# Performance work log

Hardware: AMD Instinct MI355X
Metric: run time of the kernel (lower is better)

Reference implementation:

```python
import jax, jax.numpy as jnp
import numpy as np

K = 9      # kernel_size
H = 6      # num_head
HD = 64    # head_dim
D = H * HD # reduced_hidden_dim = 384
B, S = 16, 1024
OUT = 384  # hidden_dim // 2


def setup_inputs() -> dict:
    key = jax.random.key(0)
    k = jax.random.split(key, 5)
    q = jax.random.normal(k[0], (B, S, D), dtype=jnp.float32)
    ks = jax.random.normal(k[1], (B, S, D), dtype=jnp.float32)
    v = jax.random.normal(k[2], (B, S, D), dtype=jnp.float32)
    Wk = jax.random.normal(k[3], (K * H, D), dtype=jnp.float32) * 0.02
    bk = jnp.zeros((K * H,), dtype=jnp.float32)
    Wp = jax.random.normal(k[4], (OUT, D), dtype=jnp.float32) * 0.02
    bp = jnp.zeros((OUT,), dtype=jnp.float32)
    return {"q": q, "ks": ks, "v": v, "Wk": Wk, "bk": bk, "Wp": Wp, "bp": bp}


def reference(q, ks, v, Wk, bk, Wp, bp):
    b, s, d = v.shape
    pad = K // 2
    # expand4conv: zero-pad along seq and gather K-wide sliding windows
    vp = jnp.pad(v, ((0, 0), (pad, pad), (0, 0)))            # [B, S+K-1, D]
    win = jnp.stack([vp[:, i:i + s] for i in range(K)], -1)  # [B, S, D, K]
    win = win.reshape(b, s, H, HD, K)                        # [B, S, H, HD, K]
    # dynamic kernel: softmax over kernel taps
    logits = jnp.einsum('bsd,od->bso', q * ks, Wk) + bk       # [B, S, K*H]
    dk = jax.nn.softmax(logits.reshape(b, s, H, K), axis=-1)  # [B, S, H, K]
    # local weighted reduction over the window
    out = jnp.einsum('bshdk,bshk->bshd', win, dk).reshape(b, s, d)
    return jnp.einsum('bsd,od->bso', out, Wp) + bp            # [B, S, OUT]
```

## Files before the change

kernel.cpp:

```cpp
#include <hip/hip_runtime.h>
#include <hip/hip_bf16.h>

#define BB 16
#define SS 1024
#define DD 384
#define HH 6
#define KK 9
#define KH 54
#define OUTD 384
#define NKT 12
#define VLD 392
#define RPB 32
#define NTH 512

typedef __attribute__((ext_vector_type(4))) float floatx4;
typedef __attribute__((ext_vector_type(8))) __bf16 bf16x8;
typedef __attribute__((ext_vector_type(4))) __bf16 bf16x4;

__global__ __launch_bounds__(256) void cast_kernel(const float* __restrict__ Wk,
                                                   const float* __restrict__ Wp,
                                                   __bf16* __restrict__ WkT,
                                                   __bf16* __restrict__ WpT) {
    int i = blockIdx.x * 256 + threadIdx.x;
    if (i < 4 * NKT * 64 * 8) {
        int e = i & 7, lane = (i >> 3) & 63, t = i >> 9;
        int kstep = t % NKT, ntile = t / NKT;
        int row = ntile * 16 + (lane & 15);
        int col = kstep * 32 + ((lane >> 4) << 3) + e;
        WkT[i] = (row < KH) ? (__bf16)Wk[row * DD + col] : (__bf16)0.0f;
    } else if (i < 24576 + 24 * NKT * 64 * 8) {
        int j = i - 24576;
        int e = j & 7, lane = (j >> 3) & 63, t = j >> 9;
        int kstep = t % NKT, ntile = t / NKT;
        int row = ntile * 16 + (lane & 15);
        int col = kstep * 32 + ((lane >> 4) << 3) + e;
        WpT[j] = (__bf16)Wp[row * DD + col];
    }
}

__global__ __launch_bounds__(NTH, 4) void fused_kernel(const float* __restrict__ q,
                                                       const float* __restrict__ ks,
                                                       const float* __restrict__ v,
                                                       const __bf16* __restrict__ WkT,
                                                       const float* __restrict__ bk,
                                                       const __bf16* __restrict__ WpT,
                                                       const float* __restrict__ bp,
                                                       float* __restrict__ out) {
    __shared__ __bf16 vqS[40 * VLD];
    __shared__ float  dkS[RPB * 56];
    __shared__ __align__(16) char uS[RPB * VLD * 2];
    float*  lgS = (float*)uS;
    __bf16* aS  = (__bf16*)uS;

    const int tid  = threadIdx.x;
    const int wave = tid >> 6;
    const int lane = tid & 63;
    const int m0   = blockIdx.x * RPB;
    const int b    = blockIdx.x >> 5;
    const int s0   = (blockIdx.x & 31) * RPB;
    const int fr   = lane & 15;
    const int fk   = (lane >> 4) * 8;
    const int col_in = lane & 15;
    const int rgrp   = (lane >> 4) * 4;

    floatx4 qv[6], kv[6], vpre[8];
    {
        const float* qb = q  + (size_t)m0 * DD;
        const float* kb = ks + (size_t)m0 * DD;
#pragma unroll
        for (int it = 0; it < 6; ++it) {
            int c = tid + it * NTH;
            int row = c / 96, col = (c % 96) * 4;
            qv[it] = *reinterpret_cast<const floatx4*>(qb + (size_t)row * DD + col);
            kv[it] = *reinterpret_cast<const floatx4*>(kb + (size_t)row * DD + col);
        }
        const float* vb = v + (size_t)b * SS * DD;
#pragma unroll
        for (int it = 0; it < 8; ++it) {
            int c = tid + it * NTH;
            int row = c / 96, col = (c % 96) * 4;
            int r = s0 + row - 4;
            int rc = r < 0 ? 0 : (r > SS - 1 ? SS - 1 : r);
            vpre[it] = *reinterpret_cast<const floatx4*>(vb + (size_t)rc * DD + col);
        }
#pragma unroll
        for (int it = 0; it < 6; ++it) {
            int c = tid + it * NTH;
            int row = c / 96, col = (c % 96) * 4;
            floatx4 pr = qv[it] * kv[it];
            bf16x4 pk = { (__bf16)pr.x, (__bf16)pr.y, (__bf16)pr.z, (__bf16)pr.w };
            *reinterpret_cast<bf16x4*>(&vqS[row * VLD + col]) = pk;
        }
    }
    __syncthreads();

    {
        const int rt = wave >> 2;
        const int nt = wave & 3;
        const __bf16* wkb = WkT + (((nt * NKT) * 64 + lane) << 3);
        bf16x8 wf0 = *reinterpret_cast<const bf16x8*>(wkb);
        bf16x8 wf1;
        floatx4 acc = {};
#pragma unroll
        for (int s = 0; s < NKT; ++s) {
            if (s + 1 < NKT) {
                const __bf16* nb = wkb + ((size_t)(s + 1) << 9);
                if ((s & 1) == 0) wf1 = *reinterpret_cast<const bf16x8*>(nb);
                else              wf0 = *reinterpret_cast<const bf16x8*>(nb);
            }
            bf16x8 af = *reinterpret_cast<const bf16x8*>(
                &vqS[(rt * 16 + fr) * VLD + s * 32 + fk]);
            acc = __builtin_amdgcn_mfma_f32_16x16x32_bf16(
                af, (s & 1) == 0 ? wf0 : wf1, acc, 0, 0, 0);
        }
#pragma unroll
        for (int r = 0; r < 4; ++r)
            lgS[(rt * 16 + rgrp + r) * 66 + nt * 16 + col_in] = acc[r];
    }
    __syncthreads();

    if (tid < RPB * HH) {
        int row = tid / HH, h = tid % HH;
        float lg[KK];
        float mx = -1e30f;
#pragma unroll
        for (int k = 0; k < KK; ++k) {
            float s = lgS[row * 66 + h * KK + k] + bk[h * KK + k];
            lg[k] = s;
            mx = fmaxf(mx, s);
        }
        float sum = 0.0f;
#pragma unroll
        for (int k = 0; k < KK; ++k) { lg[k] = __expf(lg[k] - mx); sum += lg[k]; }
        float inv = 1.0f / sum;
#pragma unroll
        for (int k = 0; k < KK; ++k) dkS[row * 56 + h * KK + k] = lg[k] * inv;
    }

    {
#pragma unroll
        for (int it = 0; it < 8; ++it) {
            int c = tid + it * NTH;
            if (c < 3840) {
                int row = c / 96, col = (c % 96) * 4;
                int r = s0 + row - 4;
                floatx4 val = vpre[it];
                if (r < 0 || r >= SS) val = floatx4{0.0f, 0.0f, 0.0f, 0.0f};
                bf16x4 vk = { (__bf16)val.x, (__bf16)val.y, (__bf16)val.z, (__bf16)val.w };
                *reinterpret_cast<bf16x4*>(&vqS[row * VLD + col]) = vk;
            }
        }
    }
    __syncthreads();

#pragma unroll
    for (int it = 0; it < 6; ++it) {
        int p = tid + it * NTH;
        int row = p / 96, c4 = p % 96;
        int h = c4 >> 4;
        const float* dkr = &dkS[row * 56 + h * KK];
        floatx4 a = {};
#pragma unroll
        for (int k = 0; k < KK; ++k) {
            bf16x4 w = *reinterpret_cast<const bf16x4*>(&vqS[(row + k) * VLD + c4 * 4]);
            floatx4 wf = { (float)w[0], (float)w[1], (float)w[2], (float)w[3] };
            a += wf * dkr[k];
        }
        bf16x4 o = { (__bf16)a.x, (__bf16)a.y, (__bf16)a.z, (__bf16)a.w };
        *reinterpret_cast<bf16x4*>(&aS[row * VLD + c4 * 4]) = o;
    }

    const int nt0 = wave * 3;
    const __bf16* wpb = WpT + (((nt0 * NKT) * 64 + lane) << 3);
    bf16x8 bfr[2][3];
#pragma unroll
    for (int j = 0; j < 3; ++j)
        bfr[0][j] = *reinterpret_cast<const bf16x8*>(wpb + ((size_t)(j * NKT) << 9));
    __syncthreads();

    {
        floatx4 acc[2][3] = {};
#pragma unroll
        for (int s = 0; s < NKT; ++s) {
            const int cur = s & 1, nxt = cur ^ 1;
            if (s + 1 < NKT) {
#pragma unroll
                for (int j = 0; j < 3; ++j)
                    bfr[nxt][j] = *reinterpret_cast<const bf16x8*>(
                        wpb + ((size_t)(j * NKT + s + 1) << 9));
            }
            bf16x8 a0 = *reinterpret_cast<const bf16x8*>(&aS[fr * VLD + s * 32 + fk]);
            bf16x8 a1 = *reinterpret_cast<const bf16x8*>(&aS[(16 + fr) * VLD + s * 32 + fk]);
#pragma unroll
            for (int j = 0; j < 3; ++j) {
                acc[0][j] = __builtin_amdgcn_mfma_f32_16x16x32_bf16(a0, bfr[cur][j], acc[0][j], 0, 0, 0);
                acc[1][j] = __builtin_amdgcn_mfma_f32_16x16x32_bf16(a1, bfr[cur][j], acc[1][j], 0, 0, 0);
            }
        }
        float* ob = out + (size_t)m0 * OUTD;
#pragma unroll
        for (int j = 0; j < 3; ++j) {
            int col = (nt0 + j) * 16 + col_in;
            float bv = bp[col];
#pragma unroll
            for (int rt = 0; rt < 2; ++rt)
#pragma unroll
                for (int r = 0; r < 4; ++r)
                    ob[(size_t)(rt * 16 + rgrp + r) * OUTD + col] = acc[rt][j][r] + bv;
        }
    }
}

extern "C" void kernel_launch(void* const* d_in, const int* in_sizes, int n_in,
                              void* d_out, int out_size, void* d_ws, size_t ws_size,
                              hipStream_t stream) {
    const float* q  = (const float*)d_in[0];
    const float* ks = (const float*)d_in[1];
    const float* v  = (const float*)d_in[2];
    const float* Wk = (const float*)d_in[3];
    const float* bk = (const float*)d_in[4];
    const float* Wp = (const float*)d_in[5];
    const float* bp = (const float*)d_in[6];
    float* out = (float*)d_out;

    __bf16* WkT = (__bf16*)d_ws;
    __bf16* WpT = (__bf16*)((char*)d_ws + 49152);

    cast_kernel<<<(24576 + 147456 + 255) / 256, 256, 0, stream>>>(Wk, Wp, WkT, WpT);
    fused_kernel<<<(BB * SS) / RPB, NTH, 0, stream>>>(q, ks, v, WkT, bk, WpT, bp, out);
}
```

Measured before the change: 122.9 us.

## Cut shared memory and registers to double occupancy of fused kernel

The q*ks product is now computed directly from global memory in MFMA fragment layout instead of being staged through shared memory. The v window is loaded and stored to LDS up front, with no register prefetch held across phases. Softmax weights reuse the logits buffer, and the local reduction results stay in registers until the v buffer can be overwritten. Together with launch bounds raised from 4 to 8 blocks per CU, this aims to cut LDS and VGPR use so more blocks fit per CU, at the cost of an extra barrier and less coalesced q/ks reads.

```diff
diff --git a/kernel.cpp b/kernel.cpp
--- a/kernel.cpp
+++ b/kernel.cpp
@@ -38,7 +38,7 @@
     }
 }
 
-__global__ __launch_bounds__(NTH, 4) void fused_kernel(const float* __restrict__ q,
+__global__ __launch_bounds__(NTH, 8) void fused_kernel(const float* __restrict__ q,
                                                        const float* __restrict__ ks,
                                                        const float* __restrict__ v,
                                                        const __bf16* __restrict__ WkT,
@@ -46,11 +46,8 @@
                                                        const __bf16* __restrict__ WpT,
                                                        const float* __restrict__ bp,
                                                        float* __restrict__ out) {
-    __shared__ __bf16 vqS[40 * VLD];
-    __shared__ float  dkS[RPB * 56];
-    __shared__ __align__(16) char uS[RPB * VLD * 2];
-    float*  lgS = (float*)uS;
-    __bf16* aS  = (__bf16*)uS;
+    __shared__ __bf16 vS[40 * VLD];
+    __shared__ float  lgS[RPB * 66];
 
     const int tid  = threadIdx.x;
     const int wave = tid >> 6;
@@ -63,40 +60,28 @@
     const int col_in = lane & 15;
     const int rgrp   = (lane >> 4) * 4;
 
-    floatx4 qv[6], kv[6], vpre[8];
     {
-        const float* qb = q  + (size_t)m0 * DD;
-        const float* kb = ks + (size_t)m0 * DD;
-#pragma unroll
-        for (int it = 0; it < 6; ++it) {
-            int c = tid + it * NTH;
-            int row = c / 96, col = (c % 96) * 4;
-            qv[it] = *reinterpret_cast<const floatx4*>(qb + (size_t)row * DD + col);
-            kv[it] = *reinterpret_cast<const floatx4*>(kb + (size_t)row * DD + col);
-        }
         const float* vb = v + (size_t)b * SS * DD;
 #pragma unroll
         for (int it = 0; it < 8; ++it) {
             int c = tid + it * NTH;
-            int row = c / 96, col = (c % 96) * 4;
-            int r = s0 + row - 4;
-            int rc = r < 0 ? 0 : (r > SS - 1 ? SS - 1 : r);
-            vpre[it] = *reinterpret_cast<const floatx4*>(vb + (size_t)rc * DD + col);
-        }
-#pragma unroll
-        for (int it = 0; it < 6; ++it) {
-            int c = tid + it * NTH;
-            int row = c / 96, col = (c % 96) * 4;
-            floatx4 pr = qv[it] * kv[it];
-            bf16x4 pk = { (__bf16)pr.x, (__bf16)pr.y, (__bf16)pr.z, (__bf16)pr.w };
-            *reinterpret_cast<bf16x4*>(&vqS[row * VLD + col]) = pk;
-        }
-    }
-    __syncthreads();
+            if (c < 3840) {
+                int row = c / 96, col = (c % 96) * 4;
+                int r = s0 + row - 4;
+                int rc = r < 0 ? 0 : (r > SS - 1 ? SS - 1 : r);
+                floatx4 val = *reinterpret_cast<const floatx4*>(vb + (size_t)rc * DD + col);
+                if (r < 0 || r >= SS) val = floatx4{0.0f, 0.0f, 0.0f, 0.0f};
+                bf16x4 vk4 = { (__bf16)val.x, (__bf16)val.y, (__bf16)val.z, (__bf16)val.w };
+                *reinterpret_cast<bf16x4*>(&vS[row * VLD + col]) = vk4;
+            }
+        }
+    }
 
     {
         const int rt = wave >> 2;
         const int nt = wave & 3;
+        const float* qrow = q  + (size_t)(m0 + rt * 16 + fr) * DD + fk;
+        const float* krow = ks + (size_t)(m0 + rt * 16 + fr) * DD + fk;
         const __bf16* wkb = WkT + (((nt * NKT) * 64 + lane) << 3);
         bf16x8 wf0 = *reinterpret_cast<const bf16x8*>(wkb);
         bf16x8 wf1;
@@ -108,8 +93,13 @@
                 if ((s & 1) == 0) wf1 = *reinterpret_cast<const bf16x8*>(nb);
                 else              wf0 = *reinterpret_cast<const bf16x8*>(nb);
             }
-            bf16x8 af = *reinterpret_cast<const bf16x8*>(
-                &vqS[(rt * 16 + fr) * VLD + s * 32 + fk]);
+            floatx4 q0 = *reinterpret_cast<const floatx4*>(qrow + s * 32);
+            floatx4 q1 = *reinterpret_cast<const floatx4*>(qrow + s * 32 + 4);
+            floatx4 k0 = *reinterpret_cast<const floatx4*>(krow + s * 32);
+            floatx4 k1 = *reinterpret_cast<const floatx4*>(krow + s * 32 + 4);
+            floatx4 p0 = q0 * k0, p1 = q1 * k1;
+            bf16x8 af = { (__bf16)p0.x, (__bf16)p0.y, (__bf16)p0.z, (__bf16)p0.w,
+                          (__bf16)p1.x, (__bf16)p1.y, (__bf16)p1.z, (__bf16)p1.w };
             acc = __builtin_amdgcn_mfma_f32_16x16x32_bf16(
                 af, (s & 1) == 0 ? wf0 : wf1, acc, 0, 0, 0);
         }
@@ -134,40 +124,25 @@
         for (int k = 0; k < KK; ++k) { lg[k] = __expf(lg[k] - mx); sum += lg[k]; }
         float inv = 1.0f / sum;
 #pragma unroll
-        for (int k = 0; k < KK; ++k) dkS[row * 56 + h * KK + k] = lg[k] * inv;
-    }
-
-    {
-#pragma unroll
-        for (int it = 0; it < 8; ++it) {
-            int c = tid + it * NTH;
-            if (c < 3840) {
-                int row = c / 96, col = (c % 96) * 4;
-                int r = s0 + row - 4;
-                floatx4 val = vpre[it];
-                if (r < 0 || r >= SS) val = floatx4{0.0f, 0.0f, 0.0f, 0.0f};
-                bf16x4 vk = { (__bf16)val.x, (__bf16)val.y, (__bf16)val.z, (__bf16)val.w };
-                *reinterpret_cast<bf16x4*>(&vqS[row * VLD + col]) = vk;
-            }
-        }
-    }
-    __syncthreads();
-
+        for (int k = 0; k < KK; ++k) lgS[row * 66 + h * KK + k] = lg[k] * inv;
+    }
+    __syncthreads();
+
+    bf16x4 aR[6];
 #pragma unroll
     for (int it = 0; it < 6; ++it) {
         int p = tid + it * NTH;
         int row = p / 96, c4 = p % 96;
         int h = c4 >> 4;
-        const float* dkr = &dkS[row * 56 + h * KK];
+        const float* dkr = &lgS[row * 66 + h * KK];
         floatx4 a = {};
 #pragma unroll
         for (int k = 0; k < KK; ++k) {
-            bf16x4 w = *reinterpret_cast<const bf16x4*>(&vqS[(row + k) * VLD + c4 * 4]);
+            bf16x4 w = *reinterpret_cast<const bf16x4*>(&vS[(row + k) * VLD + c4 * 4]);
             floatx4 wf = { (float)w[0], (float)w[1], (float)w[2], (float)w[3] };
             a += wf * dkr[k];
         }
-        bf16x4 o = { (__bf16)a.x, (__bf16)a.y, (__bf16)a.z, (__bf16)a.w };
-        *reinterpret_cast<bf16x4*>(&aS[row * VLD + c4 * 4]) = o;
+        aR[it] = bf16x4{ (__bf16)a.x, (__bf16)a.y, (__bf16)a.z, (__bf16)a.w };
     }
 
     const int nt0 = wave * 3;
@@ -176,6 +151,15 @@
 #pragma unroll
     for (int j = 0; j < 3; ++j)
         bfr[0][j] = *reinterpret_cast<const bf16x8*>(wpb + ((size_t)(j * NKT) << 9));
+
+    __syncthreads();
+
+#pragma unroll
+    for (int it = 0; it < 6; ++it) {
+        int p = tid + it * NTH;
+        int row = p / 96, c4 = p % 96;
+        *reinterpret_cast<bf16x4*>(&vS[row * VLD + c4 * 4]) = aR[it];
+    }
     __syncthreads();
 
     {
@@ -189,8 +173,8 @@
                     bfr[nxt][j] = *reinterpret_cast<const bf16x8*>(
                         wpb + ((size_t)(j * NKT + s + 1) << 9));
             }
-            bf16x8 a0 = *reinterpret_cast<const bf16x8*>(&aS[fr * VLD + s * 32 + fk]);
-            bf16x8 a1 = *reinterpret_cast<const bf16x8*>(&aS[(16 + fr) * VLD + s * 32 + fk]);
+            bf16x8 a0 = *reinterpret_cast<const bf16x8*>(&vS[fr * VLD + s * 32 + fk]);
+            bf16x8 a1 = *reinterpret_cast<const bf16x8*>(&vS[(16 + fr) * VLD + s * 32 + fk]);
 #pragma unroll
             for (int j = 0; j < 3; ++j) {
                 acc[0][j] = __builtin_amdgcn_mfma_f32_16x16x32_bf16(a0, bfr[cur][j], acc[0][j], 0, 0, 0);
```

After: 141.4 us. 1.15x slower.
